# Kernel optimization log

Measured on AMD Instinct MI355X. Metric: run time of the kernel, lower is better.

The kernel has to match this reference:

```python
import jax, jax.numpy as jnp
import numpy as np

B, S, D, E = 16, 2048, 1024, 1024
NEG = -1e13  # not_mask_sign from the original module


def setup_inputs() -> dict:
    key = jax.random.key(0)
    k1, k2, k3, k4, k5, k6 = jax.random.split(key, 6)
    return {
        "Q": jax.random.normal(k1, (B, S, D), dtype=jnp.float32),
        "K": jax.random.normal(k2, (B, S, D), dtype=jnp.float32),
        "V": jax.random.normal(k3, (B, S, D), dtype=jnp.float32),
        "pad_idxs": jax.random.randint(k4, (B,), 0, S, dtype=jnp.int64),
        "W": jax.random.normal(k5, (D, E), dtype=jnp.float32) * (1.0 / np.sqrt(D)),
        "b": jax.random.normal(k6, (E,), dtype=jnp.float32) * 0.01,
    }


def reference(Q, K, V, pad_idxs, W, b):
    d = Q.shape[2]
    # [B, S, S] attention scores
    scores = jnp.einsum("bqd,bkd->bqk", Q, K) / jnp.sqrt(jnp.asarray(d, Q.dtype))
    # Faithful to original: mask entries where row>=pad AND col>=pad
    idx = jnp.arange(scores.shape[1])
    p = pad_idxs[:, None, None]
    mask = (idx[None, :, None] >= p) & (idx[None, None, :] >= p)  # [B,S,S]
    scores = jnp.where(mask, jnp.asarray(NEG, scores.dtype), scores)
    attn = jax.nn.softmax(scores, axis=2)
    out = jnp.einsum("bqk,bkd->bqd", attn, V)
    return out @ W + b
```

## Files before the change

### kernel.cpp

```cpp
#include <hip/hip_runtime.h>

typedef unsigned short u16;
typedef unsigned int u32;
typedef long long ll;
typedef __attribute__((ext_vector_type(8))) short bf16x8;
typedef __attribute__((ext_vector_type(8))) unsigned short u16x8;
typedef __attribute__((ext_vector_type(4))) float f32x4;

__device__ __forceinline__ u16 f2bf(float f) {
  u32 x = __float_as_uint(f);
  x += 0x7fffu + ((x >> 16) & 1u);
  return (u16)(x >> 16);
}
__device__ __forceinline__ float bf2f(u16 u) {
  return __uint_as_float(((u32)u) << 16);
}

__device__ __forceinline__ int read_pad(const int* pw, int z) {
  int odd = pw[1] | pw[3] | pw[5] | pw[7] | pw[9] | pw[11] | pw[13] | pw[15];
  return (odd == 0) ? pw[2 * z] : pw[z];
}

template<int EPI>
__global__ __launch_bounds__(256, 4) void g128(
    const u16* __restrict__ A, const u16* __restrict__ B, void* __restrict__ C,
    int Kdim, int lda, int ldb, int ldc, ll sA, ll sB, ll sC,
    const int* __restrict__ pad, const float* __restrict__ bias,
    float* __restrict__ lsum, int NX, int NXY, int nwg) {
  __shared__ __align__(16) u16 As[128 * 64];
  __shared__ __align__(16) u16 Bs[128 * 64];

  const int orig = blockIdx.x;
  const int q8 = nwg >> 3, r8 = nwg & 7;
  const int xcd = orig & 7, inner = orig >> 3;
  const int wg = (xcd < r8 ? xcd * (q8 + 1) : r8 * (q8 + 1) + (xcd - r8) * q8) + inner;
  const int z = wg / NXY;
  const int rem = wg - z * NXY;
  const int by = rem / NX;
  const int bx = rem - by * NX;

  const int tid = threadIdx.x;
  const int wid = tid >> 6, lane = tid & 63;
  const int lr = lane & 15, lg = lane >> 4;
  const int wm = (wid >> 1) * 64, wn = (wid & 1) * 64;
  const int bm = by * 128, bn = bx * 128;
  const u16* Ab = A + (ll)z * sA + (ll)bm * lda;
  const u16* Bb = B + (ll)z * sB + (ll)bn * ldb;

  f32x4 acc[4][4];
#pragma unroll
  for (int i = 0; i < 4; ++i)
#pragma unroll
    for (int j = 0; j < 4; ++j) acc[i][j] = (f32x4)0.0f;

  const int NT = Kdim >> 6;
  for (int t = 0; t < NT; ++t) {
    __syncthreads();
#pragma unroll
    for (int i = 0; i < 4; ++i) {
      const int chunk = i * 256 + tid;
      const int r = chunk >> 3;
      const int slot = chunk & 7;
      const int gk = t * 64 + ((slot ^ (r & 7)) * 8);
      __builtin_amdgcn_global_load_lds(
          (const __attribute__((address_space(1))) void*)(Ab + (ll)r * lda + gk),
          (__attribute__((address_space(3))) void*)(As + chunk * 8), 16, 0, 0);
      __builtin_amdgcn_global_load_lds(
          (const __attribute__((address_space(1))) void*)(Bb + (ll)r * ldb + gk),
          (__attribute__((address_space(3))) void*)(Bs + chunk * 8), 16, 0, 0);
    }
    __syncthreads();
#pragma unroll
    for (int kk = 0; kk < 2; ++kk) {
      bf16x8 av[4], bv[4];
#pragma unroll
      for (int i = 0; i < 4; ++i) {
        const int ra = wm + i * 16 + lr;
        av[i] = *(const bf16x8*)(As + ra * 64 + (((kk * 4 + lg) ^ (ra & 7)) * 8));
        const int rb = wn + i * 16 + lr;
        bv[i] = *(const bf16x8*)(Bs + rb * 64 + (((kk * 4 + lg) ^ (rb & 7)) * 8));
      }
#pragma unroll
      for (int i = 0; i < 4; ++i)
#pragma unroll
        for (int j = 0; j < 4; ++j)
          acc[i][j] = __builtin_amdgcn_mfma_f32_16x16x32_bf16(av[i], bv[j],
                                                              acc[i][j], 0, 0, 0);
    }
  }

  int p = 0;
  if constexpr (EPI == 0) p = read_pad(pad, z);
#pragma unroll
  for (int mf = 0; mf < 4; ++mf) {
#pragma unroll
    for (int rg = 0; rg < 4; ++rg) {
      const int row = bm + wm + mf * 16 + 4 * lg + rg;
      if constexpr (EPI == 0) {
        float part = 0.0f;
#pragma unroll
        for (int nf = 0; nf < 4; ++nf) {
          const int col = bn + wn + nf * 16 + lr;
          float e;
          if (row >= p && col >= p) e = (p == 0) ? 1.0f : 0.0f;
          else e = __expf(acc[mf][nf][rg] * 0.03125f);
          part += e;
          ((u16*)C)[(ll)z * sC + (ll)row * ldc + col] = f2bf(e);
        }
        part += __shfl_xor(part, 1);
        part += __shfl_xor(part, 2);
        part += __shfl_xor(part, 4);
        part += __shfl_xor(part, 8);
        if (lr == 0) atomicAdd(&lsum[z * 2048 + row], part);
      } else if constexpr (EPI == 3) {
        const float linv = 1.0f / lsum[z * 2048 + row];
#pragma unroll
        for (int nf = 0; nf < 4; ++nf) {
          const int col = bn + wn + nf * 16 + lr;
          ((u16*)C)[(ll)z * sC + (ll)row * ldc + col] =
              f2bf(acc[mf][nf][rg] * linv);
        }
      } else {
#pragma unroll
        for (int nf = 0; nf < 4; ++nf) {
          const int col = bn + wn + nf * 16 + lr;
          if constexpr (EPI == 1) {
            ((u16*)C)[(ll)z * sC + (ll)row * ldc + col] = f2bf(acc[mf][nf][rg]);
          } else {
            ((float*)C)[(ll)z * sC + (ll)row * ldc + col] =
                acc[mf][nf][rg] + bias[col];
          }
        }
      }
    }
  }
}

__global__ __launch_bounds__(256) void zerof(float* __restrict__ p) {
  p[blockIdx.x * 256 + threadIdx.x] = 0.0f;
}

__global__ __launch_bounds__(256) void cvt_bf16(const float* __restrict__ src,
                                                u16* __restrict__ dst) {
  const ll i = ((ll)blockIdx.x * 256 + threadIdx.x) * 8;
  const float4 a = *(const float4*)(src + i);
  const float4 b = *(const float4*)(src + i + 4);
  u16x8 v;
  v[0] = f2bf(a.x); v[1] = f2bf(a.y); v[2] = f2bf(a.z); v[3] = f2bf(a.w);
  v[4] = f2bf(b.x); v[5] = f2bf(b.y); v[6] = f2bf(b.z); v[7] = f2bf(b.w);
  *(u16x8*)(dst + i) = v;
}

__global__ __launch_bounds__(256) void transpose_cvt(
    const float* __restrict__ src, u16* __restrict__ dst, int R, int C,
    ll sS, ll sD) {
  __shared__ u16 t[64][65];
  const int tid = threadIdx.x;
  const int r0 = blockIdx.y * 64, c0 = blockIdx.x * 64;
  const float* s = src + (ll)blockIdx.z * sS;
  u16* d = dst + (ll)blockIdx.z * sD;
#pragma unroll
  for (int it = 0; it < 16; ++it) {
    const int idx = it * 256 + tid;
    const int r = idx >> 6, c = idx & 63;
    t[r][c] = f2bf(s[(ll)(r0 + r) * C + c0 + c]);
  }
  __syncthreads();
#pragma unroll
  for (int it = 0; it < 16; ++it) {
    const int idx = it * 256 + tid;
    const int rr = idx >> 6, cc = idx & 63;
    d[(ll)(c0 + rr) * R + r0 + cc] = t[cc][rr];
  }
}

__global__ __launch_bounds__(256) void softmax_rows(u16* __restrict__ P,
                                                    const int* __restrict__ pad) {
  const int wid = threadIdx.x >> 6, lane = threadIdx.x & 63;
  const ll row = (ll)blockIdx.x * 4 + wid;
  const int z = (int)(row >> 11);
  const int r = (int)(row & 2047);
  const int p = read_pad(pad, z);
  const bool rmask = (r >= p);
  u16* ptr = P + row * 2048;
  float s[32];
#pragma unroll
  for (int i = 0; i < 4; ++i) {
    const u16x8 v = *(const u16x8*)(ptr + i * 512 + lane * 8);
#pragma unroll
    for (int j = 0; j < 8; ++j) {
      const int col = i * 512 + lane * 8 + j;
      float x = bf2f(v[j]) * 0.03125f;
      if (rmask && col >= p) x = -1e13f;
      s[i * 8 + j] = x;
    }
  }
  float m = s[0];
#pragma unroll
  for (int i = 1; i < 32; ++i) m = fmaxf(m, s[i]);
#pragma unroll
  for (int o = 1; o < 64; o <<= 1) m = fmaxf(m, __shfl_xor(m, o));
  float sum = 0.0f;
#pragma unroll
  for (int i = 0; i < 32; ++i) {
    s[i] = __expf(s[i] - m);
    sum += s[i];
  }
#pragma unroll
  for (int o = 1; o < 64; o <<= 1) sum += __shfl_xor(sum, o);
  const float inv = 1.0f / sum;
#pragma unroll
  for (int i = 0; i < 4; ++i) {
    u16x8 v;
#pragma unroll
    for (int j = 0; j < 8; ++j) v[j] = f2bf(s[i * 8 + j] * inv);
    *(u16x8*)(ptr + i * 512 + lane * 8) = v;
  }
}

__device__ __forceinline__ void stage_f32(const float* src, ll base, int ld,
                                          u16* lds, int tid) {
#pragma unroll
  for (int p = 0; p < 4; ++p) {
    int chunk = p * 256 + tid;
    int r = chunk >> 3, slot = chunk & 7;
    const float* s = src + base + (ll)r * ld + slot * 8;
    const float4 a = *(const float4*)s;
    const float4 b = *(const float4*)(s + 4);
    u16x8 v;
    v[0] = f2bf(a.x); v[1] = f2bf(a.y); v[2] = f2bf(a.z); v[3] = f2bf(a.w);
    v[4] = f2bf(b.x); v[5] = f2bf(b.y); v[6] = f2bf(b.z); v[7] = f2bf(b.w);
    *(u16x8*)(lds + r * 64 + (slot ^ (r & 7)) * 8) = v;
  }
}

__global__ __launch_bounds__(256) void gemm_f32in(
    const float* __restrict__ A, const float* __restrict__ B,
    u16* __restrict__ C, int Kdim, int lda, int ldb, int ldc,
    ll sA, ll sB, ll sC) {
  __shared__ __align__(16) u16 As[128 * 64];
  __shared__ __align__(16) u16 Bs[128 * 64];
  const int tid = threadIdx.x;
  const int z = blockIdx.z;
  const int bm = blockIdx.y * 128, bn = blockIdx.x * 128;
  const ll abase = (ll)z * sA + (ll)bm * lda;
  const ll bbase = (ll)z * sB + (ll)bn * ldb;
  const int wid = tid >> 6, lane = tid & 63;
  const int wm = (wid >> 1) * 64, wn = (wid & 1) * 64;
  const int lr = lane & 15, lg = lane >> 4;

  f32x4 acc[4][4];
#pragma unroll
  for (int i = 0; i < 4; ++i)
#pragma unroll
    for (int j = 0; j < 4; ++j) acc[i][j] = (f32x4)0.0f;

  for (int k0 = 0; k0 < Kdim; k0 += 64) {
    __syncthreads();
    stage_f32(A, abase + k0, lda, As, tid);
    stage_f32(B, bbase + k0, ldb, Bs, tid);
    __syncthreads();
#pragma unroll
    for (int kk = 0; kk < 2; ++kk) {
      bf16x8 av[4], bv[4];
#pragma unroll
      for (int i = 0; i < 4; ++i) {
        const int ra = wm + i * 16 + lr;
        av[i] = *(const bf16x8*)(As + ra * 64 + (((kk * 4 + lg) ^ (ra & 7)) * 8));
        const int rb = wn + i * 16 + lr;
        bv[i] = *(const bf16x8*)(Bs + rb * 64 + (((kk * 4 + lg) ^ (rb & 7)) * 8));
      }
#pragma unroll
      for (int i = 0; i < 4; ++i)
#pragma unroll
        for (int j = 0; j < 4; ++j)
          acc[i][j] = __builtin_amdgcn_mfma_f32_16x16x32_bf16(av[i], bv[j],
                                                              acc[i][j], 0, 0, 0);
    }
  }
#pragma unroll
  for (int i = 0; i < 4; ++i) {
    const int rowb = bm + wm + i * 16 + 4 * lg;
#pragma unroll
    for (int j = 0; j < 4; ++j) {
      const int col = bn + wn + j * 16 + lr;
#pragma unroll
      for (int rg = 0; rg < 4; ++rg)
        C[(ll)z * sC + (ll)(rowb + rg) * ldc + col] = f2bf(acc[i][j][rg]);
    }
  }
}

extern "C" void kernel_launch(void* const* d_in, const int* in_sizes, int n_in,
                              void* d_out, int out_size, void* d_ws,
                              size_t ws_size, hipStream_t stream) {
  const float* Q = (const float*)d_in[0];
  const float* Km = (const float*)d_in[1];
  const float* V = (const float*)d_in[2];
  const int* pad = (const int*)d_in[3];
  const float* W = (const float*)d_in[4];
  const float* bias = (const float*)d_in[5];
  float* out = (float*)d_out;

  const int B = 16, S = 2048, D = 1024, E = 1024;
  const ll SS = (ll)S * S, SD = (ll)S * D;

  u16* P = (u16*)d_out;
  char* ws = (char*)d_ws;

  const size_t MB64 = (size_t)B * S * D * 2;
  const size_t szWt = (size_t)D * E * 2;
  const size_t szL = (size_t)B * S * 4;

  if (ws_size >= 3 * MB64 + szWt + szL) {
    u16* Qb = (u16*)ws;
    u16* Kb = (u16*)(ws + MB64);
    u16* Vt = (u16*)(ws + 2 * MB64);
    u16* Wt = (u16*)(ws + 3 * MB64);
    float* lsum = (float*)(ws + 3 * MB64 + szWt);
    u16* X = Qb;

    const int nv = (int)(((ll)B * S * D) / (8 * 256));
    zerof<<<dim3(B * S / 256), 256, 0, stream>>>(lsum);
    cvt_bf16<<<nv, 256, 0, stream>>>(Q, Qb);
    cvt_bf16<<<nv, 256, 0, stream>>>(Km, Kb);
    transpose_cvt<<<dim3(D / 64, S / 64, B), 256, 0, stream>>>(V, Vt, S, D, SD, SD);
    transpose_cvt<<<dim3(E / 64, D / 64, 1), 256, 0, stream>>>(W, Wt, D, E, 0, 0);

    g128<0><<<dim3(4096), 256, 0, stream>>>(
        Qb, Kb, P, D, D, D, S, SD, SD, SS, pad, nullptr, lsum, 16, 256, 4096);
    g128<3><<<dim3(2048), 256, 0, stream>>>(
        P, Vt, X, S, S, S, D, SS, SD, SD, nullptr, nullptr, lsum, 8, 128, 2048);
    g128<2><<<dim3(2048), 256, 0, stream>>>(
        X, Wt, out, D, D, D, E, 0, 0, 0, nullptr, bias, nullptr, 8, 2048, 2048);
  } else if (ws_size >= 2 * MB64 + szWt) {
    u16* Vt = (u16*)ws;
    u16* Wt = (u16*)(ws + MB64);
    u16* X = (u16*)(ws + MB64 + szWt);

    transpose_cvt<<<dim3(D / 64, S / 64, B), 256, 0, stream>>>(V, Vt, S, D, SD, SD);
    transpose_cvt<<<dim3(E / 64, D / 64, 1), 256, 0, stream>>>(W, Wt, D, E, 0, 0);
    gemm_f32in<<<dim3(S / 128, S / 128, B), 256, 0, stream>>>(
        Q, Km, P, D, D, D, S, SD, SD, SS);
    softmax_rows<<<dim3(B * S / 4), 256, 0, stream>>>(P, pad);
    g128<1><<<dim3(2048), 256, 0, stream>>>(
        P, Vt, X, S, S, S, D, SS, SD, SD, nullptr, nullptr, nullptr, 8, 128, 2048);
    g128<2><<<dim3(2048), 256, 0, stream>>>(
        X, Wt, out, D, D, D, E, 0, 0, 0, nullptr, bias, nullptr, 8, 2048, 2048);
  } else {
    u16* Wt = (u16*)ws;
    u16* Vtb = (u16*)(ws + szWt);
    u16* X = (u16*)(ws + szWt + (size_t)D * S * 2);

    transpose_cvt<<<dim3(E / 64, D / 64, 1), 256, 0, stream>>>(W, Wt, D, E, 0, 0);
    gemm_f32in<<<dim3(S / 128, S / 128, B), 256, 0, stream>>>(
        Q, Km, P, D, D, D, S, SD, SD, SS);
    softmax_rows<<<dim3(B * S / 4), 256, 0, stream>>>(P, pad);
    for (int b = 0; b < B; ++b) {
      transpose_cvt<<<dim3(D / 64, S / 64, 1), 256, 0, stream>>>(
          V + (ll)b * SD, Vtb, S, D, 0, 0);
      g128<1><<<dim3(128), 256, 0, stream>>>(
          P + (ll)b * SS, Vtb, X + (ll)b * SD, S, S, S, D, 0, 0, 0, nullptr,
          nullptr, nullptr, 8, 128, 128);
    }
    g128<2><<<dim3(2048), 256, 0, stream>>>(
        X, Wt, out, D, D, D, E, 0, 0, 0, nullptr, bias, nullptr, 8, 2048, 2048);
  }
}
```

Before: 532.7 us.

## Pre-swizzle operands into MFMA fragment layout and drop LDS staging in GEMMs

Conversion kernels now write Q, K, V^T and W^T in a fragment-major layout: each 16x32 MFMA fragment sits in 512 contiguous bf16 values, one 16-byte load per lane. The GEMM becomes gfrag, which reads fragments straight from global memory into registers with double-buffered prefetch, removing the LDS tile loads and the barriers. The softmax and PV epilogues write P and X in the same fragment layout, so the chained GEMMs consume them directly. The cost is that there is no LDS reuse across waves, so each wave reloads its operands from L2/global memory, and launch bounds drop to 3 waves per SIMD to make room for the extra registers.

```diff
diff --git a/kernel.cpp b/kernel.cpp
--- a/kernel.cpp
+++ b/kernel.cpp
@@ -21,15 +21,13 @@
   return (odd == 0) ? pw[2 * z] : pw[z];
 }
 
+
 template<int EPI>
-__global__ __launch_bounds__(256, 4) void g128(
+__global__ __launch_bounds__(256, 3) void gfrag(
     const u16* __restrict__ A, const u16* __restrict__ B, void* __restrict__ C,
-    int Kdim, int lda, int ldb, int ldc, ll sA, ll sB, ll sC,
+    int KS, int KSo, int ldc, ll sA, ll sB, ll sC,
     const int* __restrict__ pad, const float* __restrict__ bias,
     float* __restrict__ lsum, int NX, int NXY, int nwg) {
-  __shared__ __align__(16) u16 As[128 * 64];
-  __shared__ __align__(16) u16 Bs[128 * 64];
-
   const int orig = blockIdx.x;
   const int q8 = nwg >> 3, r8 = nwg & 7;
   const int xcd = orig & 7, inner = orig >> 3;
@@ -39,6 +37,210 @@
   const int by = rem / NX;
   const int bx = rem - by * NX;
 
+  const int tid = threadIdx.x;
+  const int wid = tid >> 6, lane = tid & 63;
+  const int lr = lane & 15, lg = lane >> 4;
+  const int mb0 = by * 8 + (wid >> 1) * 4;
+  const int nb0 = bx * 8 + (wid & 1) * 4;
+  const u16* Ap = A + (ll)z * sA + (ll)mb0 * KS * 512 + lane * 8;
+  const u16* Bp = B + (ll)z * sB + (ll)nb0 * KS * 512 + lane * 8;
+
+  f32x4 acc[4][4];
+#pragma unroll
+  for (int i = 0; i < 4; ++i)
+#pragma unroll
+    for (int j = 0; j < 4; ++j) acc[i][j] = (f32x4)0.0f;
+
+  bf16x8 a0[4], b0[4], a1[4], b1[4];
+#pragma unroll
+  for (int i = 0; i < 4; ++i) {
+    a0[i] = *(const bf16x8*)(Ap + (ll)i * KS * 512);
+    b0[i] = *(const bf16x8*)(Bp + (ll)i * KS * 512);
+  }
+#pragma unroll
+  for (int i = 0; i < 4; ++i) {
+    a1[i] = *(const bf16x8*)(Ap + ((ll)i * KS + 1) * 512);
+    b1[i] = *(const bf16x8*)(Bp + ((ll)i * KS + 1) * 512);
+  }
+  for (int ks = 0; ks < KS - 2; ks += 2) {
+#pragma unroll
+    for (int i = 0; i < 4; ++i)
+#pragma unroll
+      for (int j = 0; j < 4; ++j)
+        acc[i][j] = __builtin_amdgcn_mfma_f32_16x16x32_bf16(a0[i], b0[j],
+                                                            acc[i][j], 0, 0, 0);
+#pragma unroll
+    for (int i = 0; i < 4; ++i) {
+      a0[i] = *(const bf16x8*)(Ap + ((ll)i * KS + ks + 2) * 512);
+      b0[i] = *(const bf16x8*)(Bp + ((ll)i * KS + ks + 2) * 512);
+    }
+#pragma unroll
+    for (int i = 0; i < 4; ++i)
+#pragma unroll
+      for (int j = 0; j < 4; ++j)
+        acc[i][j] = __builtin_amdgcn_mfma_f32_16x16x32_bf16(a1[i], b1[j],
+                                                            acc[i][j], 0, 0, 0);
+#pragma unroll
+    for (int i = 0; i < 4; ++i) {
+      a1[i] = *(const bf16x8*)(Ap + ((ll)i * KS + ks + 3) * 512);
+      b1[i] = *(const bf16x8*)(Bp + ((ll)i * KS + ks + 3) * 512);
+    }
+  }
+#pragma unroll
+  for (int i = 0; i < 4; ++i)
+#pragma unroll
+    for (int j = 0; j < 4; ++j)
+      acc[i][j] = __builtin_amdgcn_mfma_f32_16x16x32_bf16(a0[i], b0[j],
+                                                          acc[i][j], 0, 0, 0);
+#pragma unroll
+  for (int i = 0; i < 4; ++i)
+#pragma unroll
+    for (int j = 0; j < 4; ++j)
+      acc[i][j] = __builtin_amdgcn_mfma_f32_16x16x32_bf16(a1[i], b1[j],
+                                                          acc[i][j], 0, 0, 0);
+
+  int p = 0;
+  if constexpr (EPI == 0) p = read_pad(pad, z);
+#pragma unroll
+  for (int mf = 0; mf < 4; ++mf) {
+#pragma unroll
+    for (int rg = 0; rg < 4; ++rg) {
+      const int row = (mb0 + mf) * 16 + 4 * lg + rg;
+      if constexpr (EPI == 0) {
+        float part = 0.0f;
+#pragma unroll
+        for (int nf = 0; nf < 4; ++nf) {
+          const int col = (nb0 + nf) * 16 + lr;
+          float e;
+          if (row >= p && col >= p) e = (p == 0) ? 1.0f : 0.0f;
+          else e = __expf(acc[mf][nf][rg] * 0.03125f);
+          part += e;
+          ((u16*)C)[(ll)z * sC + ((ll)(row >> 4) * KSo + (col >> 5)) * 512 +
+                    (((row & 15) | (((col >> 3) & 3) << 4)) << 3) + (col & 7)] =
+              f2bf(e);
+        }
+        part += __shfl_xor(part, 1);
+        part += __shfl_xor(part, 2);
+        part += __shfl_xor(part, 4);
+        part += __shfl_xor(part, 8);
+        if (lr == 0) atomicAdd(&lsum[z * 2048 + row], part);
+      } else if constexpr (EPI == 3) {
+        const float linv = 1.0f / lsum[z * 2048 + row];
+#pragma unroll
+        for (int nf = 0; nf < 4; ++nf) {
+          const int col = (nb0 + nf) * 16 + lr;
+          ((u16*)C)[(ll)z * sC + ((ll)(row >> 4) * KSo + (col >> 5)) * 512 +
+                    (((row & 15) | (((col >> 3) & 3) << 4)) << 3) + (col & 7)] =
+              f2bf(acc[mf][nf][rg] * linv);
+        }
+      } else {
+#pragma unroll
+        for (int nf = 0; nf < 4; ++nf) {
+          const int col = (nb0 + nf) * 16 + lr;
+          ((float*)C)[(ll)row * ldc + col] = acc[mf][nf][rg] + bias[col];
+        }
+      }
+    }
+  }
+}
+
+__global__ __launch_bounds__(256) void zerof(float* __restrict__ p) {
+  p[blockIdx.x * 256 + threadIdx.x] = 0.0f;
+}
+
+__global__ __launch_bounds__(256) void cvtA_frag(const float* __restrict__ src,
+                                                 u16* __restrict__ dst) {
+  __shared__ u16 t[16 * 1032];
+  const int tid = threadIdx.x;
+  const ll rb = (ll)blockIdx.x * 16;
+#pragma unroll
+  for (int it = 0; it < 8; ++it) {
+    const int ch = it * 256 + tid;
+    const int r = ch >> 7, kc = (ch & 127) * 8;
+    const float4 a = *(const float4*)(src + (rb + r) * 1024 + kc);
+    const float4 b = *(const float4*)(src + (rb + r) * 1024 + kc + 4);
+    u16x8 v;
+    v[0] = f2bf(a.x); v[1] = f2bf(a.y); v[2] = f2bf(a.z); v[3] = f2bf(a.w);
+    v[4] = f2bf(b.x); v[5] = f2bf(b.y); v[6] = f2bf(b.z); v[7] = f2bf(b.w);
+    *(u16x8*)(t + r * 1032 + kc) = v;
+  }
+  __syncthreads();
+#pragma unroll
+  for (int it = 0; it < 8; ++it) {
+    const int fl = it * 256 + tid;
+    const int ks = fl >> 6, l = fl & 63;
+    const u16x8 v = *(const u16x8*)(t + (l & 15) * 1032 + ks * 32 + (l >> 4) * 8);
+    *(u16x8*)(dst + ((ll)blockIdx.x * 32 + ks) * 512 + l * 8) = v;
+  }
+}
+
+__global__ __launch_bounds__(256) void transpose_frag(
+    const float* __restrict__ src, u16* __restrict__ dst, int R, int C,
+    ll sS, ll sD) {
+  __shared__ u16 t[64][65];
+  const int tid = threadIdx.x;
+  const int r0 = blockIdx.y * 64, c0 = blockIdx.x * 64;
+  const float* s = src + (ll)blockIdx.z * sS;
+  u16* d = dst + (ll)blockIdx.z * sD;
+#pragma unroll
+  for (int it = 0; it < 16; ++it) {
+    const int idx = it * 256 + tid;
+    const int r = idx >> 6, c = idx & 63;
+    t[r][c] = f2bf(s[(ll)(r0 + r) * C + c0 + c]);
+  }
+  __syncthreads();
+  const int KSo = R >> 5;
+#pragma unroll
+  for (int it = 0; it < 2; ++it) {
+    const int fl = it * 256 + tid;
+    const int f = fl >> 6, l = fl & 63;
+    const int db = f >> 1, ss = f & 1;
+    u16x8 v;
+#pragma unroll
+    for (int e = 0; e < 8; ++e)
+      v[e] = t[ss * 32 + (l >> 4) * 8 + e][db * 16 + (l & 15)];
+    *(u16x8*)(d + ((ll)((c0 >> 4) + db) * KSo + ((r0 >> 5) + ss)) * 512 + l * 8) = v;
+  }
+}
+
+__global__ __launch_bounds__(256) void transpose_cvt(
+    const float* __restrict__ src, u16* __restrict__ dst, int R, int C,
+    ll sS, ll sD) {
+  __shared__ u16 t[64][65];
+  const int tid = threadIdx.x;
+  const int r0 = blockIdx.y * 64, c0 = blockIdx.x * 64;
+  const float* s = src + (ll)blockIdx.z * sS;
+  u16* d = dst + (ll)blockIdx.z * sD;
+#pragma unroll
+  for (int it = 0; it < 16; ++it) {
+    const int idx = it * 256 + tid;
+    const int r = idx >> 6, c = idx & 63;
+    t[r][c] = f2bf(s[(ll)(r0 + r) * C + c0 + c]);
+  }
+  __syncthreads();
+#pragma unroll
+  for (int it = 0; it < 16; ++it) {
+    const int idx = it * 256 + tid;
+    const int rr = idx >> 6, cc = idx & 63;
+    d[(ll)(c0 + rr) * R + r0 + cc] = t[cc][rr];
+  }
+}
+
+template<int EPI>
+__global__ __launch_bounds__(256, 4) void g128(
+    const u16* __restrict__ A, const u16* __restrict__ B, void* __restrict__ C,
+    int Kdim, int lda, int ldb, int ldc, ll sA, ll sB, ll sC,
+    const float* __restrict__ bias, int NX, int NXY, int nwg) {
+  __shared__ __align__(16) u16 As[128 * 64];
+  __shared__ __align__(16) u16 Bs[128 * 64];
+  const int orig = blockIdx.x;
+  const int q8 = nwg >> 3, r8 = nwg & 7;
+  const int xcd = orig & 7, inner = orig >> 3;
+  const int wg = (xcd < r8 ? xcd * (q8 + 1) : r8 * (q8 + 1) + (xcd - r8) * q8) + inner;
+  const int z = wg / NXY;
+  const int rem = wg - z * NXY;
+  const int by = rem / NX;
+  const int bx = rem - by * NX;
   const int tid = threadIdx.x;
   const int wid = tid >> 6, lane = tid & 63;
   const int lr = lane & 15, lg = lane >> 4;
@@ -88,89 +290,22 @@
                                                               acc[i][j], 0, 0, 0);
     }
   }
-
-  int p = 0;
-  if constexpr (EPI == 0) p = read_pad(pad, z);
 #pragma unroll
   for (int mf = 0; mf < 4; ++mf) {
 #pragma unroll
     for (int rg = 0; rg < 4; ++rg) {
       const int row = bm + wm + mf * 16 + 4 * lg + rg;
-      if constexpr (EPI == 0) {
-        float part = 0.0f;
-#pragma unroll
-        for (int nf = 0; nf < 4; ++nf) {
-          const int col = bn + wn + nf * 16 + lr;
-          float e;
-          if (row >= p && col >= p) e = (p == 0) ? 1.0f : 0.0f;
-          else e = __expf(acc[mf][nf][rg] * 0.03125f);
-          part += e;
-          ((u16*)C)[(ll)z * sC + (ll)row * ldc + col] = f2bf(e);
-        }
-        part += __shfl_xor(part, 1);
-        part += __shfl_xor(part, 2);
-        part += __shfl_xor(part, 4);
-        part += __shfl_xor(part, 8);
-        if (lr == 0) atomicAdd(&lsum[z * 2048 + row], part);
-      } else if constexpr (EPI == 3) {
-        const float linv = 1.0f / lsum[z * 2048 + row];
-#pragma unroll
-        for (int nf = 0; nf < 4; ++nf) {
-          const int col = bn + wn + nf * 16 + lr;
-          ((u16*)C)[(ll)z * sC + (ll)row * ldc + col] =
-              f2bf(acc[mf][nf][rg] * linv);
-        }
-      } else {
-#pragma unroll
-        for (int nf = 0; nf < 4; ++nf) {
-          const int col = bn + wn + nf * 16 + lr;
-          if constexpr (EPI == 1) {
-            ((u16*)C)[(ll)z * sC + (ll)row * ldc + col] = f2bf(acc[mf][nf][rg]);
-          } else {
-            ((float*)C)[(ll)z * sC + (ll)row * ldc + col] =
-                acc[mf][nf][rg] + bias[col];
-          }
+#pragma unroll
+      for (int nf = 0; nf < 4; ++nf) {
+        const int col = bn + wn + nf * 16 + lr;
+        if constexpr (EPI == 1) {
+          ((u16*)C)[(ll)z * sC + (ll)row * ldc + col] = f2bf(acc[mf][nf][rg]);
+        } else {
+          ((float*)C)[(ll)z * sC + (ll)row * ldc + col] =
+              acc[mf][nf][rg] + bias[col];
         }
       }
     }
-  }
-}
-
-__global__ __launch_bounds__(256) void zerof(float* __restrict__ p) {
-  p[blockIdx.x * 256 + threadIdx.x] = 0.0f;
-}
-
-__global__ __launch_bounds__(256) void cvt_bf16(const float* __restrict__ src,
-                                                u16* __restrict__ dst) {
-  const ll i = ((ll)blockIdx.x * 256 + threadIdx.x) * 8;
-  const float4 a = *(const float4*)(src + i);
-  const float4 b = *(const float4*)(src + i + 4);
-  u16x8 v;
-  v[0] = f2bf(a.x); v[1] = f2bf(a.y); v[2] = f2bf(a.z); v[3] = f2bf(a.w);
-  v[4] = f2bf(b.x); v[5] = f2bf(b.y); v[6] = f2bf(b.z); v[7] = f2bf(b.w);
-  *(u16x8*)(dst + i) = v;
-}
-
-__global__ __launch_bounds__(256) void transpose_cvt(
-    const float* __restrict__ src, u16* __restrict__ dst, int R, int C,
-    ll sS, ll sD) {
-  __shared__ u16 t[64][65];
-  const int tid = threadIdx.x;
-  const int r0 = blockIdx.y * 64, c0 = blockIdx.x * 64;
-  const float* s = src + (ll)blockIdx.z * sS;
-  u16* d = dst + (ll)blockIdx.z * sD;
-#pragma unroll
-  for (int it = 0; it < 16; ++it) {
-    const int idx = it * 256 + tid;
-    const int r = idx >> 6, c = idx & 63;
-    t[r][c] = f2bf(s[(ll)(r0 + r) * C + c0 + c]);
-  }
-  __syncthreads();
-#pragma unroll
-  for (int it = 0; it < 16; ++it) {
-    const int idx = it * 256 + tid;
-    const int rr = idx >> 6, cc = idx & 63;
-    d[(ll)(c0 + rr) * R + r0 + cc] = t[cc][rr];
   }
 }
 
@@ -320,19 +455,18 @@
     float* lsum = (float*)(ws + 3 * MB64 + szWt);
     u16* X = Qb;
 
-    const int nv = (int)(((ll)B * S * D) / (8 * 256));
     zerof<<<dim3(B * S / 256), 256, 0, stream>>>(lsum);
-    cvt_bf16<<<nv, 256, 0, stream>>>(Q, Qb);
-    cvt_bf16<<<nv, 256, 0, stream>>>(Km, Kb);
-    transpose_cvt<<<dim3(D / 64, S / 64, B), 256, 0, stream>>>(V, Vt, S, D, SD, SD);
-    transpose_cvt<<<dim3(E / 64, D / 64, 1), 256, 0, stream>>>(W, Wt, D, E, 0, 0);
-
-    g128<0><<<dim3(4096), 256, 0, stream>>>(
-        Qb, Kb, P, D, D, D, S, SD, SD, SS, pad, nullptr, lsum, 16, 256, 4096);
-    g128<3><<<dim3(2048), 256, 0, stream>>>(
-        P, Vt, X, S, S, S, D, SS, SD, SD, nullptr, nullptr, lsum, 8, 128, 2048);
-    g128<2><<<dim3(2048), 256, 0, stream>>>(
-        X, Wt, out, D, D, D, E, 0, 0, 0, nullptr, bias, nullptr, 8, 2048, 2048);
+    cvtA_frag<<<dim3(B * S / 16), 256, 0, stream>>>(Q, Qb);
+    cvtA_frag<<<dim3(B * S / 16), 256, 0, stream>>>(Km, Kb);
+    transpose_frag<<<dim3(D / 64, S / 64, B), 256, 0, stream>>>(V, Vt, S, D, SD, SD);
+    transpose_frag<<<dim3(E / 64, D / 64, 1), 256, 0, stream>>>(W, Wt, D, E, 0, 0);
+
+    gfrag<0><<<dim3(4096), 256, 0, stream>>>(
+        Qb, Kb, P, 32, 64, 0, SD, SD, SS, pad, nullptr, lsum, 16, 256, 4096);
+    gfrag<3><<<dim3(2048), 256, 0, stream>>>(
+        P, Vt, X, 64, 32, 0, SS, SD, SD, nullptr, nullptr, lsum, 8, 128, 2048);
+    gfrag<2><<<dim3(2048), 256, 0, stream>>>(
+        X, Wt, out, 32, 0, E, 0, 0, 0, nullptr, bias, nullptr, 8, 2048, 2048);
   } else if (ws_size >= 2 * MB64 + szWt) {
     u16* Vt = (u16*)ws;
     u16* Wt = (u16*)(ws + MB64);
@@ -341,12 +475,12 @@
     transpose_cvt<<<dim3(D / 64, S / 64, B), 256, 0, stream>>>(V, Vt, S, D, SD, SD);
     transpose_cvt<<<dim3(E / 64, D / 64, 1), 256, 0, stream>>>(W, Wt, D, E, 0, 0);
     gemm_f32in<<<dim3(S / 128, S / 128, B), 256, 0, stream>>>(
-        Q, Km, P, D, D, D, S, SD, SD, SS);
-    softmax_rows<<<dim3(B * S / 4), 256, 0, stream>>>(P, pad);
+        Q, Km, (u16*)d_out, D, D, D, S, SD, SD, SS);
+    softmax_rows<<<dim3(B * S / 4), 256, 0, stream>>>((u16*)d_out, pad);
     g128<1><<<dim3(2048), 256, 0, stream>>>(
-        P, Vt, X, S, S, S, D, SS, SD, SD, nullptr, nullptr, nullptr, 8, 128, 2048);
+        (u16*)d_out, Vt, X, S, S, S, D, SS, SD, SD, nullptr, 8, 128, 2048);
     g128<2><<<dim3(2048), 256, 0, stream>>>(
-        X, Wt, out, D, D, D, E, 0, 0, 0, nullptr, bias, nullptr, 8, 2048, 2048);
+        X, Wt, out, D, D, D, E, 0, 0, 0, bias, 8, 2048, 2048);
   } else {
     u16* Wt = (u16*)ws;
     u16* Vtb = (u16*)(ws + szWt);
@@ -354,16 +488,16 @@
 
     transpose_cvt<<<dim3(E / 64, D / 64, 1), 256, 0, stream>>>(W, Wt, D, E, 0, 0);
     gemm_f32in<<<dim3(S / 128, S / 128, B), 256, 0, stream>>>(
-        Q, Km, P, D, D, D, S, SD, SD, SS);
-    softmax_rows<<<dim3(B * S / 4), 256, 0, stream>>>(P, pad);
+        Q, Km, (u16*)d_out, D, D, D, S, SD, SD, SS);
+    softmax_rows<<<dim3(B * S / 4), 256, 0, stream>>>((u16*)d_out, pad);
     for (int b = 0; b < B; ++b) {
       transpose_cvt<<<dim3(D / 64, S / 64, 1), 256, 0, stream>>>(
           V + (ll)b * SD, Vtb, S, D, 0, 0);
       g128<1><<<dim3(128), 256, 0, stream>>>(
-          P + (ll)b * SS, Vtb, X + (ll)b * SD, S, S, S, D, 0, 0, 0, nullptr,
-          nullptr, nullptr, 8, 128, 128);
+          (u16*)d_out + (ll)b * SS, Vtb, X + (ll)b * SD, S, S, S, D, 0, 0, 0,
+          nullptr, 8, 128, 128);
     }
     g128<2><<<dim3(2048), 256, 0, stream>>>(
-        X, Wt, out, D, D, D, E, 0, 0, 0, nullptr, bias, nullptr, 8, 2048, 2048);
-  }
-}
+        X, Wt, out, D, D, D, E, 0, 0, 0, bias, 8, 2048, 2048);
+  }
+}
```

New measurement: 670.8 us. 25.9% more time.
